# Performance work log

Measured on AMD Instinct MI355X. Metric: run time of the kernel, lower is better.

The kernel has to match this reference:

```python
import jax, jax.numpy as jnp
import numpy as np

N = 100_000          # nodes
E = 3_200_000        # edges (avg degree 32)
USER_SIZE = 80_000
CAT_SIZE = 5_000
USER_DIM = 8
CAT_DIM = 4
IN_CH = 8
OUT_CH = 16
HID = 16


def setup_inputs() -> dict:
    key = jax.random.key(0)
    ks = jax.random.split(key, 24)
    # features: [N,3] int; col0 = id (user id if type==0 else category id), col1 = known flag in {0,1}, col2 = type in {0,1}
    typ = jax.random.randint(ks[0], (N,), 0, 2)
    uid = jax.random.randint(ks[1], (N,), 0, USER_SIZE)
    cid = jax.random.randint(ks[2], (N,), 0, CAT_SIZE)
    col0 = jnp.where(typ == 0, uid, cid)
    col1 = jax.random.randint(ks[3], (N,), 0, 2)
    features = jnp.stack([col0, col1, typ], axis=1).astype(jnp.int64)
    edges = jax.random.randint(ks[4], (2, E), 0, N).astype(jnp.int64)

    def p(k, shape):
        return jax.random.normal(k, shape, dtype=jnp.float32) * 0.1

    return {
        "edges": edges,
        "features": features,
        "emb_user": p(ks[5], (USER_SIZE, USER_DIM)),
        "emb_known": p(ks[6], (2, USER_DIM)),
        "w_user": p(ks[7], (USER_DIM, IN_CH)),
        "b_user": p(ks[8], (IN_CH,)),
        "emb_cat": p(ks[9], (CAT_SIZE, CAT_DIM)),
        "w_cat": p(ks[10], (CAT_DIM, IN_CH)),
        "b_cat": p(ks[11], (IN_CH,)),
        "w0": p(ks[12], (IN_CH, HID)),
        "b0": p(ks[13], (HID,)),
        "w2": p(ks[14], (HID, OUT_CH)),
        "b2": p(ks[15], (OUT_CH,)),
        "w_node": p(ks[16], (OUT_CH, 2)),
        "b_node": p(ks[17], (2,)),
        "w_mem": p(ks[18], (OUT_CH, 1)),
        "b_mem": p(ks[19], (1,)),
    }


def _gcn_conv(x, w, b, src, dst, edge_norm, self_norm, n):
    h = x @ w                                      # [N, out]
    msgs = h[src] * edge_norm[:, None]             # [E, out] gather + scale
    agg = jax.ops.segment_sum(msgs, dst, num_segments=n)  # scatter-add
    agg = agg + h * self_norm[:, None]             # self-loop term
    return agg + b


def reference(edges, features, emb_user, emb_known, w_user, b_user, emb_cat,
              w_cat, b_cat, w0, b0, w2, b2, w_node, b_node, w_mem, b_mem):
    n = features.shape[0]
    typ = features[:, -1]
    is_user = (typ == 0)

    # --- input encoding (masked gather/scatter expressed as dense select) ---
    uidx = jnp.clip(features[:, 0], 0, emb_user.shape[0] - 1)
    kidx = jnp.clip(features[:, 1], 0, 1)
    cidx = jnp.clip(features[:, 0], 0, emb_cat.shape[0] - 1)
    user_f = jax.nn.relu(emb_user[uidx] + emb_known[kidx]) @ w_user + b_user
    cat_f = jax.nn.relu(emb_cat[cidx]) @ w_cat + b_cat
    x = jnp.where(is_user[:, None], user_f, cat_f)  # [N, IN_CH]

    # --- GCN normalization (shared across layers) ---
    src, dst = edges[0], edges[1]
    deg = jax.ops.segment_sum(jnp.ones((src.shape[0],), x.dtype), dst,
                              num_segments=n) + 1.0  # +1 for self-loop
    dinv = jax.lax.rsqrt(deg)
    edge_norm = dinv[src] * dinv[dst]
    self_norm = dinv * dinv

    # NOTE: original forward loop skips layers[1] entirely (enumerate over layers[:-2],
    # then applies layers[-1]); dropout branch (i>1) never triggers. Faithful here.
    h = jax.nn.relu(_gcn_conv(x, w0, b0, src, dst, edge_norm, self_norm, n))
    h = jax.nn.relu(_gcn_conv(h, w2, b2, src, dst, edge_norm, self_norm, n))

    member_pred = h @ w_mem + b_mem   # [N, 1]
    node_pred = h @ w_node + b_node   # [N, 2]
    return (member_pred, node_pred)
```

## Files before the change

kernel.cpp:

```cpp
#include <hip/hip_runtime.h>
#include <hip/hip_fp16.h>

#define BLK 256
#define PBLK 1024
#define NPB 256
#define CSHIFT 10
#define CNODES 1024
#define CMASK 1023
#define NBCMAX 128
#define CAP 40960
#define SSHIFT 6
#define NSL 16
#define SROWS 64
#define SRMASK 63
#define NCHK 8
#define FCAP2 384
#define FXS 1048576.0f
#define FXI (1.0f / 1048576.0f)
#define PBIAS (1 << 23)

typedef int v4i __attribute__((ext_vector_type(4)));
typedef unsigned long long u64;

static inline int cdiv(int a, int b) { return (a + b - 1) / b; }

__global__ void __launch_bounds__(PBLK)
k_part(const int* __restrict__ src, const int* __restrict__ dst,
       int* __restrict__ gcur, int* __restrict__ slab, int e, int nb) {
    __shared__ int hist[4][NBCMAX];
    __shared__ int curs[NBCMAX];
    __shared__ int rend[NBCMAX];
    int tid = threadIdx.x;
    int rep = (tid >> 6) & 3;
    for (int t = tid; t < 4 * NBCMAX; t += PBLK) ((int*)hist)[t] = 0;
    __syncthreads();
    int per = ((e + (int)gridDim.x - 1) / (int)gridDim.x + 3) & ~3;
    int beg = blockIdx.x * per;
    int end = min(e, beg + per);
    if (beg < end) {
        int m4 = beg + ((end - beg) & ~3);
        for (int i = beg + tid * 4; i < m4; i += PBLK * 4) {
            v4i d4 = *reinterpret_cast<const v4i*>(dst + i);
            atomicAdd(&hist[rep][d4[0] >> CSHIFT], 1);
            atomicAdd(&hist[rep][d4[1] >> CSHIFT], 1);
            atomicAdd(&hist[rep][d4[2] >> CSHIFT], 1);
            atomicAdd(&hist[rep][d4[3] >> CSHIFT], 1);
        }
        int it = m4 + tid;
        if (it < end) atomicAdd(&hist[rep][dst[it] >> CSHIFT], 1);
    }
    __syncthreads();
    for (int b = tid; b < nb; b += PBLK) {
        int cnt = hist[0][b] + hist[1][b] + hist[2][b] + hist[3][b];
        int r16 = (cnt + 15) & ~15;
        int base = 0;
        if (r16) base = atomicAdd(&gcur[b], r16);
        int a0 = b * CAP + min(base, CAP);
        int a1 = b * CAP + min(base + r16, CAP);
        curs[b] = a0;
        rend[b] = a1;
    }
    __syncthreads();
    if (beg < end) {
        int m4 = beg + ((end - beg) & ~3);
        for (int i = beg + tid * 4; i < m4; i += PBLK * 4) {
            v4i s4 = *reinterpret_cast<const v4i*>(src + i);
            v4i d4 = *reinterpret_cast<const v4i*>(dst + i);
#pragma unroll
            for (int k = 0; k < 4; ++k) {
                int d = d4[k];
                int b = d >> CSHIFT;
                int pos = atomicAdd(&curs[b], 1);
                if (pos < rend[b]) slab[pos] = (s4[k] << CSHIFT) | (d & CMASK);
            }
        }
        int it = m4 + tid;
        if (it < end) {
            int d = dst[it];
            int b = d >> CSHIFT;
            int pos = atomicAdd(&curs[b], 1);
            if (pos < rend[b]) slab[pos] = (src[it] << CSHIFT) | (d & CMASK);
        }
    }
    __syncthreads();
    for (int b = tid; b < nb; b += PBLK) {
        for (int x = curs[b]; x < rend[b]; ++x) slab[x] = -1;
    }
}

__global__ void __launch_bounds__(PBLK)
k_refine(const int* __restrict__ tot, const int* __restrict__ cslab,
         int* __restrict__ fslab, int* __restrict__ ftot,
         int* __restrict__ deg, int n) {
    __shared__ int cur[NSL];
    __shared__ int cnt[CNODES];
    int tid = threadIdx.x;
    int b = blockIdx.x >> 3;
    int p = blockIdx.x & 7;
    if (tid < NSL) cur[tid] = 0;
    for (int t = tid; t < CNODES; t += PBLK) cnt[t] = 0;
    __syncthreads();
    int nlines = min(tot[b], CAP) >> 4;
    int q0 = ((p * nlines) >> 3) << 2;
    int q1 = (((p + 1) * nlines) >> 3) << 2;
    const v4i* sl4 = reinterpret_cast<const v4i*>(cslab + (size_t)b * CAP);
    for (int i = q0 + tid; i < q1; i += PBLK) {
        v4i e4 = sl4[i];
#pragma unroll
        for (int k = 0; k < 4; ++k) {
            int e = e4[k];
            if (e >= 0) {
                int s = (e >> SSHIFT) & (NSL - 1);
                int fe = ((e >> CSHIFT) << SSHIFT) | (e & SRMASK);
                atomicAdd(&cnt[e & CMASK], 1);
                int pos = atomicAdd(&cur[s], 1);
                if (pos < FCAP2) fslab[(size_t)((b * NSL + s) * NCHK + p) * FCAP2 + pos] = fe;
            }
        }
    }
    __syncthreads();
    if (tid < NSL) {
        int cc = min(cur[tid], FCAP2);
        int r = min((cc + 15) & ~15, FCAP2);
        int* seg = fslab + (size_t)((b * NSL + tid) * NCHK + p) * FCAP2;
        for (int x = cc; x < r; ++x) seg[x] = -1;
        ftot[(b * NSL + tid) * NCHK + p] = r;
    }
    for (int t = tid; t < CNODES; t += PBLK) {
        int v = cnt[t];
        int nd = b * CNODES + t;
        if (v && nd < n) atomicAdd(&deg[nd], v);
    }
}

__global__ void k_featmm(const int* __restrict__ feat,
                         const float* __restrict__ emb_user,
                         const float* __restrict__ emb_known,
                         const float* __restrict__ w_user,
                         const float* __restrict__ b_user,
                         const float* __restrict__ emb_cat,
                         const float* __restrict__ w_cat,
                         const float* __restrict__ b_cat,
                         const float* __restrict__ w0,
                         const int* __restrict__ deg,
                         __half* __restrict__ Hs,
                         int n, int user_max, int cat_max) {
    __shared__ float w0s[8 * 16];
    for (int t = threadIdx.x; t < 8 * 16; t += blockDim.x) w0s[t] = w0[t];
    __syncthreads();
    int i = blockIdx.x * blockDim.x + threadIdx.x;
    if (i >= n) return;
    int col0 = feat[i * 3 + 0];
    int col1 = feat[i * 3 + 1];
    int typ  = feat[i * 3 + 2];
    float x[8];
    if (typ == 0) {
        int u = min(max(col0, 0), user_max);
        int k = min(max(col1, 0), 1);
        const float4* eu = reinterpret_cast<const float4*>(emb_user + (size_t)u * 8);
        const float4* ek = reinterpret_cast<const float4*>(emb_known + (size_t)k * 8);
        float4 a0 = eu[0], a1 = eu[1], k0 = ek[0], k1 = ek[1];
        float in[8];
        in[0] = fmaxf(a0.x + k0.x, 0.f); in[1] = fmaxf(a0.y + k0.y, 0.f);
        in[2] = fmaxf(a0.z + k0.z, 0.f); in[3] = fmaxf(a0.w + k0.w, 0.f);
        in[4] = fmaxf(a1.x + k1.x, 0.f); in[5] = fmaxf(a1.y + k1.y, 0.f);
        in[6] = fmaxf(a1.z + k1.z, 0.f); in[7] = fmaxf(a1.w + k1.w, 0.f);
#pragma unroll
        for (int c = 0; c < 8; ++c) {
            float s = b_user[c];
#pragma unroll
            for (int d = 0; d < 8; ++d) s += in[d] * w_user[d * 8 + c];
            x[c] = s;
        }
    } else {
        int ci = min(max(col0, 0), cat_max);
        float4 c0 = reinterpret_cast<const float4*>(emb_cat + (size_t)ci * 4)[0];
        float in[4];
        in[0] = fmaxf(c0.x, 0.f); in[1] = fmaxf(c0.y, 0.f);
        in[2] = fmaxf(c0.z, 0.f); in[3] = fmaxf(c0.w, 0.f);
#pragma unroll
        for (int c = 0; c < 8; ++c) {
            float s = b_cat[c];
#pragma unroll
            for (int d = 0; d < 4; ++d) s += in[d] * w_cat[d * 8 + c];
            x[c] = s;
        }
    }
    float dv = rsqrtf((float)deg[i] + 1.0f);
    float o[16];
#pragma unroll
    for (int c = 0; c < 16; ++c) {
        float s = 0.f;
#pragma unroll
        for (int d = 0; d < 8; ++d) s += x[d] * w0s[d * 16 + c];
        o[c] = s * dv;
    }
    union { __half2 h[8]; uint4 u[2]; } pk;
#pragma unroll
    for (int k = 0; k < 8; ++k) pk.h[k] = __floats2half2_rn(o[2 * k], o[2 * k + 1]);
    uint4* dp = reinterpret_cast<uint4*>(Hs + (size_t)i * 16);
    dp[0] = pk.u[0];
    dp[1] = pk.u[1];
}

__device__ __forceinline__ void gather_pair(const int* __restrict__ run0, int n0,
                                            const int* __restrict__ run1, int n1,
                                            const uint4* __restrict__ Hs4,
                                            u64 (*acc64)[9], int tid) {
    const v4i* sl0 = reinterpret_cast<const v4i*>(run0);
    const v4i* sl1 = reinterpret_cast<const v4i*>(run1);
    int ns0 = n0 >> 2, ns1 = n1 >> 2;
    int maxs = max(ns0, ns1);
    int g = tid >> 1, q = tid & 1;
    for (int base = 0; base < maxs; base += 128) {
        int i = base + g;
        v4i e0 = sl0[min(i, (FCAP2 >> 2) - 1)];
        v4i e1 = sl1[min(i, (FCAP2 >> 2) - 1)];
        bool b0 = i < ns0, b1 = i < ns1;
        int us[8];
        us[0] = b0 ? e0[0] : -1; us[1] = b0 ? e0[1] : -1;
        us[2] = b0 ? e0[2] : -1; us[3] = b0 ? e0[3] : -1;
        us[4] = b1 ? e1[0] : -1; us[5] = b1 ? e1[1] : -1;
        us[6] = b1 ? e1[2] : -1; us[7] = b1 ? e1[3] : -1;
        uint4 v[8];
#pragma unroll
        for (int k = 0; k < 8; ++k)
            if (us[k] >= 0) v[k] = Hs4[(size_t)(us[k] >> SSHIFT) * 2 + q];
#pragma unroll
        for (int k = 0; k < 8; ++k) {
            if (us[k] >= 0) {
                int dl = us[k] & SRMASK;
                union { uint4 u4; __half2 h[4]; } c;
                c.u4 = v[k];
#pragma unroll
                for (int j = 0; j < 4; ++j) {
                    float2 f = __half22float2(c.h[j]);
                    unsigned a0 = (unsigned)(__float2int_rn(f.x * FXS) + PBIAS);
                    unsigned a1 = (unsigned)(__float2int_rn(f.y * FXS) + PBIAS);
                    u64 pk = ((u64)a1 << 32) | (u64)a0;
                    atomicAdd(&acc64[dl][q * 4 + j], pk);
                }
            }
        }
    }
}

__device__ __forceinline__ void gather_fb(const int* __restrict__ ftot,
                                          const int* __restrict__ fslab,
                                          int fb, const uint4* __restrict__ Hs4,
                                          u64 (*acc64)[9], int tid) {
#pragma unroll
    for (int p = 0; p < NCHK; p += 2) {
        const int* r0 = fslab + (size_t)(fb * NCHK + p) * FCAP2;
        const int* r1 = fslab + (size_t)(fb * NCHK + p + 1) * FCAP2;
        gather_pair(r0, ftot[fb * NCHK + p], r1, ftot[fb * NCHK + p + 1], Hs4, acc64, tid);
    }
}

__device__ __forceinline__ float unpack_acc(const u64 (*acc64)[9], int node, int c, int dg) {
    u64 w = acc64[node][c >> 1];
    unsigned raw = (c & 1) ? (unsigned)(w >> 32) : (unsigned)(w & 0xffffffffULL);
    long long t = (long long)raw - (long long)dg * PBIAS;
    return (float)t * FXI;
}

__global__ void __launch_bounds__(BLK, 8)
k_bconv1(const int* __restrict__ ftot, const int* __restrict__ fslab,
         const __half* __restrict__ Hs, const int* __restrict__ deg,
         const float* __restrict__ b0, const float* __restrict__ w2,
         __half* __restrict__ Hs2, int n) {
    __shared__ u64 acc64[SROWS][9];
    __shared__ float w2s[16 * 16];
    __shared__ float b0s[16];
    int tid = threadIdx.x;
    for (int t = tid; t < SROWS * 9; t += BLK) ((u64*)acc64)[t] = 0ull;
    w2s[tid] = w2[tid];
    if (tid < 16) b0s[tid] = b0[tid];
    __syncthreads();
    int fb = blockIdx.x;
    gather_fb(ftot, fslab, fb, reinterpret_cast<const uint4*>(Hs), acc64, tid);
    __syncthreads();
    int node = tid & 63;
    int qq = tid >> 6;
    int nd = (fb >> 4) * CNODES + (fb & (NSL - 1)) * SROWS + node;
    if (nd < n) {
        int dg = deg[nd];
        float dv = rsqrtf((float)dg + 1.0f);
        const __half* hrow = Hs + (size_t)nd * 16;
        float h1[16];
#pragma unroll
        for (int c = 0; c < 16; ++c) {
            float v = dv * (unpack_acc(acc64, node, c, dg) + __half2float(hrow[c])) + b0s[c];
            h1[c] = v > 0.f ? v : 0.f;
        }
        float o[4];
#pragma unroll
        for (int j = 0; j < 4; ++j) {
            float sum = 0.f;
#pragma unroll
            for (int c = 0; c < 16; ++c) sum += h1[c] * w2s[c * 16 + qq * 4 + j];
            o[j] = sum * dv;
        }
        union { __half2 h[2]; uint2 u; } pk;
        pk.h[0] = __floats2half2_rn(o[0], o[1]);
        pk.h[1] = __floats2half2_rn(o[2], o[3]);
        *reinterpret_cast<uint2*>(Hs2 + (size_t)nd * 16 + qq * 4) = pk.u;
    }
}

__global__ void __launch_bounds__(BLK, 8)
k_bconv2(const int* __restrict__ ftot, const int* __restrict__ fslab,
         const __half* __restrict__ Hs, const int* __restrict__ deg,
         const float* __restrict__ b2,
         const float* __restrict__ w_mem, const float* __restrict__ b_mem,
         const float* __restrict__ w_node, const float* __restrict__ b_node,
         float* __restrict__ out, int n) {
    __shared__ u64 acc64[SROWS][9];
    __shared__ float wms[16], wn0[16], wn1[16], b2s[16];
    int tid = threadIdx.x;
    for (int t = tid; t < SROWS * 9; t += BLK) ((u64*)acc64)[t] = 0ull;
    if (tid < 16) {
        wms[tid] = w_mem[tid];
        wn0[tid] = w_node[tid * 2 + 0];
        wn1[tid] = w_node[tid * 2 + 1];
        b2s[tid] = b2[tid];
    }
    __syncthreads();
    int fb = blockIdx.x;
    gather_fb(ftot, fslab, fb, reinterpret_cast<const uint4*>(Hs), acc64, tid);
    __syncthreads();
    int nd = (fb >> 4) * CNODES + (fb & (NSL - 1)) * SROWS + tid;
    if (tid < SROWS && nd < n) {
        int dg = deg[nd];
        float dv = rsqrtf((float)dg + 1.0f);
        const __half* hrow = Hs + (size_t)nd * 16;
        float mph = b_mem[0];
        float n0 = b_node[0];
        float n1 = b_node[1];
#pragma unroll
        for (int c = 0; c < 16; ++c) {
            float v = dv * (unpack_acc(acc64, tid, c, dg) + __half2float(hrow[c])) + b2s[c];
            float h = v > 0.f ? v : 0.f;
            mph += h * wms[c];
            n0  += h * wn0[c];
            n1  += h * wn1[c];
        }
        out[nd] = mph;
        out[n + 2 * nd + 0] = n0;
        out[n + 2 * nd + 1] = n1;
    }
}

extern "C" void kernel_launch(void* const* d_in, const int* in_sizes, int n_in,
                              void* d_out, int out_size, void* d_ws, size_t ws_size,
                              hipStream_t stream) {
    const int*   edges     = (const int*)d_in[0];
    const int*   feat      = (const int*)d_in[1];
    const float* emb_user  = (const float*)d_in[2];
    const float* emb_known = (const float*)d_in[3];
    const float* w_user    = (const float*)d_in[4];
    const float* b_user    = (const float*)d_in[5];
    const float* emb_cat   = (const float*)d_in[6];
    const float* w_cat     = (const float*)d_in[7];
    const float* b_cat     = (const float*)d_in[8];
    const float* w0        = (const float*)d_in[9];
    const float* b0        = (const float*)d_in[10];
    const float* w2        = (const float*)d_in[11];
    const float* b2        = (const float*)d_in[12];
    const float* w_node    = (const float*)d_in[13];
    const float* b_node    = (const float*)d_in[14];
    const float* w_mem     = (const float*)d_in[15];
    const float* b_mem     = (const float*)d_in[16];

    const int E = in_sizes[0] / 2;
    const int n = in_sizes[1] / 3;
    const int user_max = in_sizes[2] / 8 - 1;
    const int cat_max  = in_sizes[6] / 4 - 1;
    const int NBC = cdiv(n, CNODES);
    const int NBF = NBC * NSL;

    const int* src = edges;
    const int* dst = edges + E;

    int* cslab   = (int*)d_ws;
    int* fslab   = cslab + (size_t)NBC * CAP;
    __half* hsA  = (__half*)(fslab + (size_t)NBF * NCHK * FCAP2);
    __half* hsB  = hsA + (size_t)n * 16;
    int* gcur    = (int*)(hsB + (size_t)n * 16);
    int* deg     = gcur + NBC;
    int* ftot    = deg + n;

    float* outp = (float*)d_out;

    hipMemsetAsync(gcur, 0, (size_t)(NBC + n) * sizeof(int), stream);
    k_part<<<NPB, PBLK, 0, stream>>>(src, dst, gcur, cslab, E, NBC);
    k_refine<<<NBC * NCHK, PBLK, 0, stream>>>(gcur, cslab, fslab, ftot, deg, n);
    k_featmm<<<cdiv(n, BLK), BLK, 0, stream>>>(feat, emb_user, emb_known, w_user, b_user,
                                               emb_cat, w_cat, b_cat, w0, deg, hsA,
                                               n, user_max, cat_max);
    k_bconv1<<<NBF, BLK, 0, stream>>>(ftot, fslab, hsA, deg, b0, w2, hsB, n);
    k_bconv2<<<NBF, BLK, 0, stream>>>(ftot, fslab, hsB, deg, b2,
                                      w_mem, b_mem, w_node, b_node, outp, n);
}
```

Before: 101.0 us.

## Software-pipeline edge slab loads across chunk pairs and enlarge NPB

```diff
diff --git a/kernel.cpp b/kernel.cpp
--- a/kernel.cpp
+++ b/kernel.cpp
@@ -3,7 +3,7 @@
 
 #define BLK 256
 #define PBLK 1024
-#define NPB 256
+#define NPB 512
 #define CSHIFT 10
 #define CNODES 1024
 #define CMASK 1023
@@ -203,20 +203,28 @@
     dp[1] = pk.u[1];
 }
 
-__device__ __forceinline__ void gather_pair(const int* __restrict__ run0, int n0,
-                                            const int* __restrict__ run1, int n1,
-                                            const uint4* __restrict__ Hs4,
-                                            u64 (*acc64)[9], int tid) {
-    const v4i* sl0 = reinterpret_cast<const v4i*>(run0);
-    const v4i* sl1 = reinterpret_cast<const v4i*>(run1);
-    int ns0 = n0 >> 2, ns1 = n1 >> 2;
-    int maxs = max(ns0, ns1);
+__device__ __forceinline__ void gather_fb(const int* __restrict__ ftot,
+                                          const int* __restrict__ fslab,
+                                          int fb, const uint4* __restrict__ Hs4,
+                                          u64 (*acc64)[9], int tid) {
+    const int LIM = (FCAP2 >> 2) - 1;
     int g = tid >> 1, q = tid & 1;
-    for (int base = 0; base < maxs; base += 128) {
-        int i = base + g;
-        v4i e0 = sl0[min(i, (FCAP2 >> 2) - 1)];
-        v4i e1 = sl1[min(i, (FCAP2 >> 2) - 1)];
-        bool b0 = i < ns0, b1 = i < ns1;
+    int gi = min(g, LIM);
+    v4i e0 = reinterpret_cast<const v4i*>(fslab + (size_t)(fb * NCHK + 0) * FCAP2)[gi];
+    v4i e1 = reinterpret_cast<const v4i*>(fslab + (size_t)(fb * NCHK + 1) * FCAP2)[gi];
+    int ns0 = ftot[fb * NCHK + 0] >> 2;
+    int ns1 = ftot[fb * NCHK + 1] >> 2;
+#pragma unroll
+    for (int p = 0; p < NCHK; p += 2) {
+        v4i f0 = e0, f1 = e1;
+        int ms0 = 0, ms1 = 0;
+        if (p + 2 < NCHK) {
+            f0 = reinterpret_cast<const v4i*>(fslab + (size_t)(fb * NCHK + p + 2) * FCAP2)[gi];
+            f1 = reinterpret_cast<const v4i*>(fslab + (size_t)(fb * NCHK + p + 3) * FCAP2)[gi];
+            ms0 = ftot[fb * NCHK + p + 2] >> 2;
+            ms1 = ftot[fb * NCHK + p + 3] >> 2;
+        }
+        bool b0 = g < ns0, b1 = g < ns1;
         int us[8];
         us[0] = b0 ? e0[0] : -1; us[1] = b0 ? e0[1] : -1;
         us[2] = b0 ? e0[2] : -1; us[3] = b0 ? e0[3] : -1;
@@ -242,18 +250,7 @@
                 }
             }
         }
-    }
-}
-
-__device__ __forceinline__ void gather_fb(const int* __restrict__ ftot,
-                                          const int* __restrict__ fslab,
-                                          int fb, const uint4* __restrict__ Hs4,
-                                          u64 (*acc64)[9], int tid) {
-#pragma unroll
-    for (int p = 0; p < NCHK; p += 2) {
-        const int* r0 = fslab + (size_t)(fb * NCHK + p) * FCAP2;
-        const int* r1 = fslab + (size_t)(fb * NCHK + p + 1) * FCAP2;
-        gather_pair(r0, ftot[fb * NCHK + p], r1, ftot[fb * NCHK + p + 1], Hs4, acc64, tid);
+        e0 = f0; e1 = f1; ns0 = ms0; ns1 = ms1;
     }
 }
 
```

Result: slower. 106.8 us (+5.7%).
